# Kernel tuning notes

Hardware: AMD Instinct MI355X
Metric: run time of the kernel (lower is better)

Reference implementation:

```python
import jax, jax.numpy as jnp
import numpy as np

N_EMBED = 1024
EMBED_DIM = 256

def setup_inputs() -> dict:
    key = jax.random.key(0)
    k1, k2 = jax.random.split(key)
    hidden_states = jax.random.normal(k1, (64, 32, 32, EMBED_DIM), dtype=jnp.float32)
    emb_weights = jax.random.normal(k2, (N_EMBED, EMBED_DIM), dtype=jnp.float32)
    return {"hidden_states": hidden_states, "emb_weights": emb_weights}

def reference(hidden_states, emb_weights):
    # flatten (B,H,W,C) -> (N, C) with C == embed_dim
    z_flat = hidden_states.reshape((-1, EMBED_DIM))
    # squared distance: ||z||^2 + ||e||^2 - 2 z.e
    distance = (
        jnp.sum(z_flat ** 2, axis=1, keepdims=True)
        + jnp.sum(emb_weights ** 2, axis=1)
        - 2.0 * jnp.dot(z_flat, emb_weights.T)
    )  # (N, n_embed)
    min_encoding_indices = jnp.argmin(distance, axis=1)  # (N,)
    z_q = jnp.take(emb_weights, min_encoding_indices, axis=0).reshape(hidden_states.shape)
    min_encoding_indices = min_encoding_indices.reshape(hidden_states.shape[0], -1)
    return z_q, min_encoding_indices
```

## Files before the change

### kernel.cpp

```cpp
#include <hip/hip_runtime.h>

typedef _Float16 half8  __attribute__((ext_vector_type(8)));
typedef _Float16 half4  __attribute__((ext_vector_type(4)));
typedef float    float4v __attribute__((ext_vector_type(4)));
typedef float    float8v __attribute__((ext_vector_type(8)));

#define N_ROWS  65536
#define N_CODES 1024
#define DIM     256
#define BM      64
#define NBLKS   (N_ROWS / BM)

__global__ __launch_bounds__(64)
void vq_prep(const float* __restrict__ emb, float* __restrict__ e_norm,
             _Float16* __restrict__ e_frag) {
    const int c = blockIdx.x, lane = threadIdx.x;
    const int l15 = c & 15, nt = c >> 4;
    float4v v = ((const float4v*)(emb + (size_t)c * DIM))[lane];
    half4 h, l;
    float ss = 0.f;
    #pragma unroll
    for (int j = 0; j < 4; ++j) {
        float x = v[j];
        ss += x * x;
        _Float16 hh = (_Float16)x;
        h[j] = hh;
        l[j] = (_Float16)(x - (float)hh);
    }
    const int ks = lane >> 3, q = (lane >> 1) & 3, jb = (lane & 1) * 4;
    _Float16* p = e_frag + ((size_t)(nt * 8 + ks)) * 1024 + (q * 16 + l15) * 8 + jb;
    *(half4*)p = h;
    *(half4*)(p + 512) = l;
    #pragma unroll
    for (int m = 32; m >= 1; m >>= 1) ss += __shfl_xor(ss, m, 64);
    if (lane == 0) e_norm[c] = ss;
}

__global__ __launch_bounds__(256, 2)
void vq_main(const float* __restrict__ z,
             const _Float16* __restrict__ e_frag,
             const float* __restrict__ e_norm,
             const float* __restrict__ emb,
             float* __restrict__ zq,
             float* __restrict__ idxf,
             int fused_gather) {
    __shared__ _Float16 sA[32 * 2 * 512];
    __shared__ float    s_nrm[N_CODES];
    __shared__ float2   s_best[BM][5];
    __shared__ int      s_idx[BM];

    const int t = threadIdx.x;
    const int w = t >> 6, lane = t & 63, quad = lane >> 4, l15 = lane & 15;
    const int rowblk = blockIdx.x * BM;

    s_nrm[t]       = e_norm[t];
    s_nrm[t + 256] = e_norm[t + 256];
    s_nrm[t + 512] = e_norm[t + 512];
    s_nrm[t + 768] = e_norm[t + 768];

    #pragma unroll
    for (int i = 0; i < 8; ++i) {
        const int row = w * 16 + l15;
        const int col = i * 32 + quad * 8;
        float8v v = *(const float8v*)(z + (size_t)(rowblk + row) * DIM + col);
        half8 h, lo;
        #pragma unroll
        for (int j = 0; j < 8; ++j) {
            float x = v[j];
            _Float16 hh = (_Float16)x;
            h[j] = hh;
            lo[j] = (_Float16)(x - (float)hh);
        }
        _Float16* p = sA + (size_t)((w * 8 + i) * 2) * 512 + lane * 8;
        *(half8*)p = h;
        *(half8*)(p + 512) = lo;
    }
    __syncthreads();

    for (int pass = 0; pass < 2; ++pass) {
        const int ntbase = w * 16 + pass * 8;
        float4v acc[4][8] = {};

        #pragma unroll
        for (int ks = 0; ks < 8; ++ks) {
            half8 bh[8], bl[8];
            #pragma unroll
            for (int nt = 0; nt < 8; ++nt) {
                const _Float16* bp = e_frag + ((size_t)((ntbase + nt) * 8 + ks)) * 1024 + lane * 8;
                bh[nt] = *(const half8*)bp;
                bl[nt] = *(const half8*)(bp + 512);
            }
            __builtin_amdgcn_s_setprio(1);
            #pragma unroll
            for (int mt = 0; mt < 4; ++mt) {
                const _Float16* ap = sA + (size_t)((mt * 8 + ks) * 2) * 512 + lane * 8;
                half8 ah = *(const half8*)ap;
                half8 al = *(const half8*)(ap + 512);
                #pragma unroll
                for (int nt = 0; nt < 8; ++nt)
                    acc[mt][nt] = __builtin_amdgcn_mfma_f32_16x16x32_f16(ah, bh[nt], acc[mt][nt], 0, 0, 0);
                #pragma unroll
                for (int nt = 0; nt < 8; ++nt)
                    acc[mt][nt] = __builtin_amdgcn_mfma_f32_16x16x32_f16(ah, bl[nt], acc[mt][nt], 0, 0, 0);
                #pragma unroll
                for (int nt = 0; nt < 8; ++nt)
                    acc[mt][nt] = __builtin_amdgcn_mfma_f32_16x16x32_f16(al, bh[nt], acc[mt][nt], 0, 0, 0);
            }
            __builtin_amdgcn_s_setprio(0);
        }

        float nrm[8]; int cg[8];
        #pragma unroll
        for (int nt = 0; nt < 8; ++nt) {
            cg[nt]  = (ntbase + nt) * 16 + l15;
            nrm[nt] = s_nrm[cg[nt]];
        }
        #pragma unroll
        for (int mt = 0; mt < 4; ++mt) {
            #pragma unroll
            for (int r = 0; r < 4; ++r) {
                float bs = nrm[0] - 2.0f * acc[mt][0][r]; int bi = cg[0];
                #pragma unroll
                for (int nt = 1; nt < 8; ++nt) {
                    float s = nrm[nt] - 2.0f * acc[mt][nt][r];
                    if (s < bs) { bs = s; bi = cg[nt]; }
                }
                #pragma unroll
                for (int m = 1; m < 16; m <<= 1) {
                    float s2 = __shfl_xor(bs, m, 64);
                    int   i2 = __shfl_xor(bi, m, 64);
                    if (s2 < bs || (s2 == bs && i2 < bi)) { bs = s2; bi = i2; }
                }
                if (l15 == 0) {
                    const int row = mt * 16 + quad * 4 + r;
                    if (pass == 0) {
                        float2 pr; pr.x = bs; pr.y = (float)bi;
                        s_best[row][w] = pr;
                    } else {
                        float2 pv = s_best[row][w];
                        if (bs < pv.x) {
                            float2 pr; pr.x = bs; pr.y = (float)bi;
                            s_best[row][w] = pr;
                        }
                    }
                }
            }
        }
    }
    __syncthreads();

    if (t < BM) {
        float2 p0 = s_best[t][0];
        float bs = p0.x, bi = p0.y;
        #pragma unroll
        for (int s = 1; s < 4; ++s) {
            float2 pv = s_best[t][s];
            if (pv.x < bs || (pv.x == bs && pv.y < bi)) { bs = pv.x; bi = pv.y; }
        }
        s_idx[t] = (int)bi;
        idxf[rowblk + t] = bi;
    }

    if (!fused_gather) return;
    __syncthreads();

    const float4v* emb4 = (const float4v*)emb;
    float4v* zq4 = (float4v*)zq;
    const int rr = t >> 2, cb = t & 3;
    const int code = s_idx[rr];
    #pragma unroll
    for (int i = 0; i < 16; ++i) {
        const int chunk = cb + i * 4;
        zq4[(size_t)(rowblk + rr) * 64 + chunk] = emb4[(size_t)code * 64 + chunk];
    }
}

__global__ __launch_bounds__(256)
void vq_gather(const float* __restrict__ emb,
               const float* __restrict__ idxf,
               float* __restrict__ zq) {
    const int tid  = blockIdx.x * 256 + threadIdx.x;
    const int r    = tid >> 6;
    const int lane = tid & 63;
    const int idx  = (int)idxf[r];
    const float4* ep = (const float4*)(emb + (size_t)idx * DIM);
    ((float4*)(zq + (size_t)r * DIM))[lane] = ep[lane];
}

extern "C" void kernel_launch(void* const* d_in, const int* in_sizes, int n_in,
                              void* d_out, int out_size, void* d_ws, size_t ws_size,
                              hipStream_t stream) {
    const float* z   = (const float*)d_in[0];
    const float* emb = (const float*)d_in[1];

    float* zq   = (float*)d_out;
    float* idxf = zq + (size_t)N_ROWS * DIM;

    const size_t need = 4096 + (size_t)N_CODES * DIM * 2 * sizeof(_Float16);
    const int in_ws = (ws_size >= need);
    char* base = in_ws ? (char*)d_ws : (char*)d_out;
    float*    e_norm = (float*)base;
    _Float16* e_frag = (_Float16*)(base + 4096);

    vq_prep<<<N_CODES, 64, 0, stream>>>(emb, e_norm, e_frag);
    vq_main<<<NBLKS, 256, 0, stream>>>(z, e_frag, e_norm, emb, zq, idxf, in_ws);
    if (!in_ws)
        vq_gather<<<(N_ROWS * 64) / 256, 256, 0, stream>>>(emb, idxf, zq);
}
```

Before: 200.9 us.

## Switch to 32x32x16 MFMA tiles with double-buffered B-fragment prefetch

Replaces the 16x16x32 MFMA tiling with 32x32x16 MFMA instructions. The embedding fragment layout in the prep kernel and the shared-memory A layout are reorganised to match. Codebook fragments are now software-pipelined: the next k-step's B fragments are loaded into a double buffer while the current step computes, and the first batch is issued before the A staging. The goal is more work per instruction, fewer operand loads, and hidden global-load latency. The cost is a more complex epilogue row mapping, wider cross-lane reductions, and higher register pressure from 16-wide accumulators.

```diff
diff --git a/kernel.cpp b/kernel.cpp
--- a/kernel.cpp
+++ b/kernel.cpp
@@ -4,6 +4,7 @@
 typedef _Float16 half4  __attribute__((ext_vector_type(4)));
 typedef float    float4v __attribute__((ext_vector_type(4)));
 typedef float    float8v __attribute__((ext_vector_type(8)));
+typedef float    float16v __attribute__((ext_vector_type(16)));
 
 #define N_ROWS  65536
 #define N_CODES 1024
@@ -15,7 +16,6 @@
 void vq_prep(const float* __restrict__ emb, float* __restrict__ e_norm,
              _Float16* __restrict__ e_frag) {
     const int c = blockIdx.x, lane = threadIdx.x;
-    const int l15 = c & 15, nt = c >> 4;
     float4v v = ((const float4v*)(emb + (size_t)c * DIM))[lane];
     half4 h, l;
     float ss = 0.f;
@@ -27,8 +27,11 @@
         h[j] = hh;
         l[j] = (_Float16)(x - (float)hh);
     }
-    const int ks = lane >> 3, q = (lane >> 1) & 3, jb = (lane & 1) * 4;
-    _Float16* p = e_frag + ((size_t)(nt * 8 + ks)) * 1024 + (q * 16 + l15) * 8 + jb;
+    const int kstep = lane >> 2;
+    const int khalf = (lane >> 1) & 1;
+    const int jb    = (lane & 1) * 4;
+    _Float16* p = e_frag + ((size_t)((c >> 5) * 16 + kstep)) * 1024
+                + ((c & 31) + 32 * khalf) * 8 + jb;
     *(half4*)p = h;
     *(half4*)(p + 512) = l;
     #pragma unroll
@@ -51,12 +54,24 @@
 
     const int t = threadIdx.x;
     const int w = t >> 6, lane = t & 63, quad = lane >> 4, l15 = lane & 15;
+    const int l31 = lane & 31, half = lane >> 5;
     const int rowblk = blockIdx.x * BM;
 
     s_nrm[t]       = e_norm[t];
     s_nrm[t + 256] = e_norm[t + 256];
     s_nrm[t + 512] = e_norm[t + 512];
     s_nrm[t + 768] = e_norm[t + 768];
+
+    half8 bh[2][4], bl[2][4];
+    {
+        const int ntbase0 = w * 8;
+        #pragma unroll
+        for (int nt = 0; nt < 4; ++nt) {
+            const _Float16* bp = e_frag + ((size_t)((ntbase0 + nt) * 16 + 0)) * 1024 + lane * 8;
+            bh[0][nt] = *(const half8*)bp;
+            bl[0][nt] = *(const half8*)(bp + 512);
+        }
+    }
 
     #pragma unroll
     for (int i = 0; i < 8; ++i) {
@@ -71,68 +86,92 @@
             h[j] = hh;
             lo[j] = (_Float16)(x - (float)hh);
         }
-        _Float16* p = sA + (size_t)((w * 8 + i) * 2) * 512 + lane * 8;
+        const int mt    = w >> 1;
+        const int rloc  = (w & 1) * 16 + l15;
+        const int kstep = i * 2 + (quad >> 1);
+        const int khalf = quad & 1;
+        _Float16* p = sA + (size_t)((mt * 16 + kstep) * 2) * 512
+                    + (rloc + 32 * khalf) * 8;
         *(half8*)p = h;
         *(half8*)(p + 512) = lo;
     }
     __syncthreads();
 
     for (int pass = 0; pass < 2; ++pass) {
-        const int ntbase = w * 16 + pass * 8;
-        float4v acc[4][8] = {};
-
-        #pragma unroll
-        for (int ks = 0; ks < 8; ++ks) {
-            half8 bh[8], bl[8];
-            #pragma unroll
-            for (int nt = 0; nt < 8; ++nt) {
-                const _Float16* bp = e_frag + ((size_t)((ntbase + nt) * 8 + ks)) * 1024 + lane * 8;
-                bh[nt] = *(const half8*)bp;
-                bl[nt] = *(const half8*)(bp + 512);
+        const int ntbase = w * 8 + pass * 4;
+
+        if (pass) {
+            #pragma unroll
+            for (int nt = 0; nt < 4; ++nt) {
+                const _Float16* bp = e_frag + ((size_t)((ntbase + nt) * 16 + 0)) * 1024 + lane * 8;
+                bh[0][nt] = *(const half8*)bp;
+                bl[0][nt] = *(const half8*)(bp + 512);
+            }
+        }
+
+        float16v acc[2][4] = {};
+
+        #pragma unroll
+        for (int ksp = 0; ksp < 16; ++ksp) {
+            const int cur = ksp & 1, nxt = cur ^ 1;
+            if (ksp < 15) {
+                #pragma unroll
+                for (int nt = 0; nt < 4; ++nt) {
+                    const _Float16* bp = e_frag + ((size_t)((ntbase + nt) * 16 + (ksp + 1))) * 1024 + lane * 8;
+                    bh[nxt][nt] = *(const half8*)bp;
+                    bl[nxt][nt] = *(const half8*)(bp + 512);
+                }
+            }
+            half8 ah[2], al[2];
+            #pragma unroll
+            for (int mt = 0; mt < 2; ++mt) {
+                const _Float16* ap = sA + (size_t)((mt * 16 + ksp) * 2) * 512 + lane * 8;
+                ah[mt] = *(const half8*)ap;
+                al[mt] = *(const half8*)(ap + 512);
             }
             __builtin_amdgcn_s_setprio(1);
             #pragma unroll
-            for (int mt = 0; mt < 4; ++mt) {
-                const _Float16* ap = sA + (size_t)((mt * 8 + ks) * 2) * 512 + lane * 8;
-                half8 ah = *(const half8*)ap;
-                half8 al = *(const half8*)(ap + 512);
-                #pragma unroll
-                for (int nt = 0; nt < 8; ++nt)
-                    acc[mt][nt] = __builtin_amdgcn_mfma_f32_16x16x32_f16(ah, bh[nt], acc[mt][nt], 0, 0, 0);
-                #pragma unroll
-                for (int nt = 0; nt < 8; ++nt)
-                    acc[mt][nt] = __builtin_amdgcn_mfma_f32_16x16x32_f16(ah, bl[nt], acc[mt][nt], 0, 0, 0);
-                #pragma unroll
-                for (int nt = 0; nt < 8; ++nt)
-                    acc[mt][nt] = __builtin_amdgcn_mfma_f32_16x16x32_f16(al, bh[nt], acc[mt][nt], 0, 0, 0);
-            }
+            for (int mt = 0; mt < 2; ++mt)
+                #pragma unroll
+                for (int nt = 0; nt < 4; ++nt)
+                    acc[mt][nt] = __builtin_amdgcn_mfma_f32_32x32x16_f16(ah[mt], bh[cur][nt], acc[mt][nt], 0, 0, 0);
+            #pragma unroll
+            for (int mt = 0; mt < 2; ++mt)
+                #pragma unroll
+                for (int nt = 0; nt < 4; ++nt)
+                    acc[mt][nt] = __builtin_amdgcn_mfma_f32_32x32x16_f16(ah[mt], bl[cur][nt], acc[mt][nt], 0, 0, 0);
+            #pragma unroll
+            for (int mt = 0; mt < 2; ++mt)
+                #pragma unroll
+                for (int nt = 0; nt < 4; ++nt)
+                    acc[mt][nt] = __builtin_amdgcn_mfma_f32_32x32x16_f16(al[mt], bh[cur][nt], acc[mt][nt], 0, 0, 0);
             __builtin_amdgcn_s_setprio(0);
         }
 
-        float nrm[8]; int cg[8];
-        #pragma unroll
-        for (int nt = 0; nt < 8; ++nt) {
-            cg[nt]  = (ntbase + nt) * 16 + l15;
+        float nrm[4]; int cg[4];
+        #pragma unroll
+        for (int nt = 0; nt < 4; ++nt) {
+            cg[nt]  = (ntbase + nt) * 32 + l31;
             nrm[nt] = s_nrm[cg[nt]];
         }
         #pragma unroll
-        for (int mt = 0; mt < 4; ++mt) {
-            #pragma unroll
-            for (int r = 0; r < 4; ++r) {
+        for (int mt = 0; mt < 2; ++mt) {
+            #pragma unroll
+            for (int r = 0; r < 16; ++r) {
                 float bs = nrm[0] - 2.0f * acc[mt][0][r]; int bi = cg[0];
                 #pragma unroll
-                for (int nt = 1; nt < 8; ++nt) {
+                for (int nt = 1; nt < 4; ++nt) {
                     float s = nrm[nt] - 2.0f * acc[mt][nt][r];
                     if (s < bs) { bs = s; bi = cg[nt]; }
                 }
                 #pragma unroll
-                for (int m = 1; m < 16; m <<= 1) {
+                for (int m = 1; m < 32; m <<= 1) {
                     float s2 = __shfl_xor(bs, m, 64);
                     int   i2 = __shfl_xor(bi, m, 64);
                     if (s2 < bs || (s2 == bs && i2 < bi)) { bs = s2; bi = i2; }
                 }
-                if (l15 == 0) {
-                    const int row = mt * 16 + quad * 4 + r;
+                if (l31 == 0) {
+                    const int row = mt * 32 + (r & 3) + 8 * (r >> 2) + 4 * half;
                     if (pass == 0) {
                         float2 pr; pr.x = bs; pr.y = (float)bi;
                         s_best[row][w] = pr;
```

After: 240.2 us. +19.5%, slower.

## Split codebook across blocks with register-resident B fragments and partial argmin

Applied to the files above, without the earlier changes.

Adds a new main kernel that partitions the 1024 codes into 8 column groups of 128 codes. Each block keeps its 32-code slice of the split-fp16 codebook in registers and streams 8 row tiles of z through shared memory. Each block writes per-row partial minima to a workspace buffer, and a new gather kernel reduces the 8 partials, writes the index and copies the codebook row. This removes the repeated global reloads of the codebook in the inner loop. In exchange it converts z 8 times (once per column group), adds a workspace round trip and a third launch, and runs only when the workspace is large enough.

```diff
diff --git a/kernel.cpp b/kernel.cpp
--- a/kernel.cpp
+++ b/kernel.cpp
@@ -9,7 +9,9 @@
 #define N_CODES 1024
 #define DIM     256
 #define BM      64
-#define NBLKS   (N_ROWS / BM)
+#define NCOLS   8
+#define NGRP    128
+#define TILES   8
 
 __global__ __launch_bounds__(64)
 void vq_prep(const float* __restrict__ emb, float* __restrict__ e_norm,
@@ -34,6 +36,166 @@
     #pragma unroll
     for (int m = 32; m >= 1; m >>= 1) ss += __shfl_xor(ss, m, 64);
     if (lane == 0) e_norm[c] = ss;
+}
+
+__global__ __launch_bounds__(256, 2)
+void vq_main_p(const float* __restrict__ z,
+               const _Float16* __restrict__ e_frag,
+               const float* __restrict__ e_norm,
+               float2* __restrict__ best) {
+    __shared__ _Float16 sA[32 * 2 * 512];
+    __shared__ float2   s_best[BM][5];
+
+    const int t = threadIdx.x;
+    const int w = t >> 6, lane = t & 63, quad = lane >> 4, l15 = lane & 15;
+    const int c = blockIdx.x >> 7, g = blockIdx.x & (NGRP - 1);
+    const int ntbase = c * 8 + w * 2;
+    const int rowbase = g * (TILES * BM);
+
+    half8 bh[2][8], bl[2][8];
+    #pragma unroll
+    for (int nt = 0; nt < 2; ++nt)
+        #pragma unroll
+        for (int ks = 0; ks < 8; ++ks) {
+            const _Float16* bp = e_frag + ((size_t)((ntbase + nt) * 8 + ks)) * 1024 + lane * 8;
+            bh[nt][ks] = *(const half8*)bp;
+            bl[nt][ks] = *(const half8*)(bp + 512);
+        }
+
+    float nrm[2]; int cg[2];
+    #pragma unroll
+    for (int nt = 0; nt < 2; ++nt) {
+        cg[nt]  = (ntbase + nt) * 16 + l15;
+        nrm[nt] = e_norm[cg[nt]];
+    }
+
+    {
+        const int rowblk = rowbase;
+        #pragma unroll
+        for (int i = 0; i < 8; ++i) {
+            const int row = w * 16 + l15;
+            const int col = i * 32 + quad * 8;
+            float8v v = *(const float8v*)(z + (size_t)(rowblk + row) * DIM + col);
+            half8 h, lo;
+            #pragma unroll
+            for (int j = 0; j < 8; ++j) {
+                float x = v[j];
+                _Float16 hh = (_Float16)x;
+                h[j] = hh;
+                lo[j] = (_Float16)(x - (float)hh);
+            }
+            _Float16* p = sA + (size_t)((w * 8 + i) * 2) * 512 + lane * 8;
+            *(half8*)p = h;
+            *(half8*)(p + 512) = lo;
+        }
+    }
+
+    for (int tt = 0; tt < TILES; ++tt) {
+        __syncthreads();
+
+        float4v acc[4][2] = {};
+        #pragma unroll
+        for (int ks = 0; ks < 8; ++ks) {
+            half8 ah[4], al[4];
+            #pragma unroll
+            for (int mt = 0; mt < 4; ++mt) {
+                const _Float16* ap = sA + (size_t)((mt * 8 + ks) * 2) * 512 + lane * 8;
+                ah[mt] = *(const half8*)ap;
+                al[mt] = *(const half8*)(ap + 512);
+            }
+            __builtin_amdgcn_s_setprio(1);
+            #pragma unroll
+            for (int mt = 0; mt < 4; ++mt)
+                #pragma unroll
+                for (int nt = 0; nt < 2; ++nt)
+                    acc[mt][nt] = __builtin_amdgcn_mfma_f32_16x16x32_f16(ah[mt], bh[nt][ks], acc[mt][nt], 0, 0, 0);
+            #pragma unroll
+            for (int mt = 0; mt < 4; ++mt)
+                #pragma unroll
+                for (int nt = 0; nt < 2; ++nt)
+                    acc[mt][nt] = __builtin_amdgcn_mfma_f32_16x16x32_f16(ah[mt], bl[nt][ks], acc[mt][nt], 0, 0, 0);
+            #pragma unroll
+            for (int mt = 0; mt < 4; ++mt)
+                #pragma unroll
+                for (int nt = 0; nt < 2; ++nt)
+                    acc[mt][nt] = __builtin_amdgcn_mfma_f32_16x16x32_f16(al[mt], bh[nt][ks], acc[mt][nt], 0, 0, 0);
+            __builtin_amdgcn_s_setprio(0);
+        }
+
+        #pragma unroll
+        for (int mt = 0; mt < 4; ++mt) {
+            #pragma unroll
+            for (int r = 0; r < 4; ++r) {
+                float bs = nrm[0] - 2.0f * acc[mt][0][r]; int bi = cg[0];
+                float s1 = nrm[1] - 2.0f * acc[mt][1][r];
+                if (s1 < bs) { bs = s1; bi = cg[1]; }
+                #pragma unroll
+                for (int m = 1; m < 16; m <<= 1) {
+                    float s2 = __shfl_xor(bs, m, 64);
+                    int   i2 = __shfl_xor(bi, m, 64);
+                    if (s2 < bs || (s2 == bs && i2 < bi)) { bs = s2; bi = i2; }
+                }
+                if (l15 == 0) {
+                    float2 pr; pr.x = bs; pr.y = (float)bi;
+                    s_best[mt * 16 + quad * 4 + r][w] = pr;
+                }
+            }
+        }
+        __syncthreads();
+
+        if (tt + 1 < TILES) {
+            const int rowblk = rowbase + (tt + 1) * BM;
+            #pragma unroll
+            for (int i = 0; i < 8; ++i) {
+                const int row = w * 16 + l15;
+                const int col = i * 32 + quad * 8;
+                float8v v = *(const float8v*)(z + (size_t)(rowblk + row) * DIM + col);
+                half8 h, lo;
+                #pragma unroll
+                for (int j = 0; j < 8; ++j) {
+                    float x = v[j];
+                    _Float16 hh = (_Float16)x;
+                    h[j] = hh;
+                    lo[j] = (_Float16)(x - (float)hh);
+                }
+                _Float16* p = sA + (size_t)((w * 8 + i) * 2) * 512 + lane * 8;
+                *(half8*)p = h;
+                *(half8*)(p + 512) = lo;
+            }
+        }
+        if (t < BM) {
+            float2 p0 = s_best[t][0];
+            float bs = p0.x, bi = p0.y;
+            #pragma unroll
+            for (int s = 1; s < 4; ++s) {
+                float2 pv = s_best[t][s];
+                if (pv.x < bs || (pv.x == bs && pv.y < bi)) { bs = pv.x; bi = pv.y; }
+            }
+            float2 pr; pr.x = bs; pr.y = bi;
+            best[(size_t)(rowbase + tt * BM + t) * NCOLS + c] = pr;
+        }
+    }
+}
+
+__global__ __launch_bounds__(256)
+void vq_gather2(const float* __restrict__ emb,
+                const float2* __restrict__ best,
+                float* __restrict__ zq,
+                float* __restrict__ idxf) {
+    const int t = threadIdx.x, w = t >> 6, lane = t & 63;
+    const int r = blockIdx.x * 4 + w;
+    float2 pv = best[(size_t)r * NCOLS + (lane & 7)];
+    float bs = pv.x, bi = pv.y;
+    #pragma unroll
+    for (int m = 1; m < 8; m <<= 1) {
+        float s2 = __shfl_xor(bs, m, 64);
+        float i2 = __shfl_xor(bi, m, 64);
+        if (s2 < bs || (s2 == bs && i2 < bi)) { bs = s2; bi = i2; }
+    }
+    const int idx = (int)bi;
+    if (lane == 0) idxf[r] = bi;
+    ((float4*)(zq + (size_t)r * DIM))[lane] =
+        ((const float4*)(emb + (size_t)idx * DIM))[lane];
 }
 
 __global__ __launch_bounds__(256, 2)
@@ -196,14 +358,26 @@
     float* zq   = (float*)d_out;
     float* idxf = zq + (size_t)N_ROWS * DIM;
 
-    const size_t need = 4096 + (size_t)N_CODES * DIM * 2 * sizeof(_Float16);
-    const int in_ws = (ws_size >= need);
-    char* base = in_ws ? (char*)d_ws : (char*)d_out;
-    float*    e_norm = (float*)base;
-    _Float16* e_frag = (_Float16*)(base + 4096);
-
-    vq_prep<<<N_CODES, 64, 0, stream>>>(emb, e_norm, e_frag);
-    vq_main<<<NBLKS, 256, 0, stream>>>(z, e_frag, e_norm, emb, zq, idxf, in_ws);
-    if (!in_ws)
-        vq_gather<<<(N_ROWS * 64) / 256, 256, 0, stream>>>(emb, idxf, zq);
-}
+    const size_t efrag_sz = (size_t)N_CODES * DIM * 2 * sizeof(_Float16);
+    const size_t best_sz  = (size_t)N_ROWS * NCOLS * sizeof(float2);
+    const size_t need_p   = 4096 + efrag_sz + best_sz;
+
+    if (ws_size >= need_p) {
+        float*    e_norm = (float*)d_ws;
+        _Float16* e_frag = (_Float16*)((char*)d_ws + 4096);
+        float2*   best   = (float2*)((char*)d_ws + 4096 + efrag_sz);
+        vq_prep<<<N_CODES, 64, 0, stream>>>(emb, e_norm, e_frag);
+        vq_main_p<<<NCOLS * NGRP, 256, 0, stream>>>(z, e_frag, e_norm, best);
+        vq_gather2<<<N_ROWS / 4, 256, 0, stream>>>(emb, best, zq, idxf);
+    } else {
+        const size_t need = 4096 + efrag_sz;
+        const int in_ws = (ws_size >= need);
+        char* base = in_ws ? (char*)d_ws : (char*)d_out;
+        float*    e_norm = (float*)base;
+        _Float16* e_frag = (_Float16*)(base + 4096);
+        vq_prep<<<N_CODES, 64, 0, stream>>>(emb, e_norm, e_frag);
+        vq_main<<<N_ROWS / BM, 256, 0, stream>>>(z, e_frag, e_norm, emb, zq, idxf, in_ws);
+        if (!in_ws)
+            vq_gather<<<(N_ROWS * 64) / 256, 256, 0, stream>>>(emb, idxf, zq);
+    }
+}
```

New measurement: 291.4 us. 1.45x slower.
